# Performance work log

Hardware: AMD Instinct MI355X
Metric: run time of the kernel (lower is better)

The kernel has to match this reference:

```python
import jax, jax.numpy as jnp
import numpy as np

D_MODEL = 1024
NHEAD = 16
DK = D_MODEL // NHEAD
B, LQ, LK = 4, 2048, 2048


def setup_inputs() -> dict:
    key = jax.random.key(0)
    ks = jax.random.split(key, 11)
    s = 1.0 / np.sqrt(D_MODEL)
    inp = {
        "q": jax.random.normal(ks[0], (B, LQ, D_MODEL), jnp.float32),
        "k": jax.random.normal(ks[1], (B, LK, D_MODEL), jnp.float32),
        "v": jax.random.normal(ks[2], (B, LK, D_MODEL), jnp.float32),
        "attn_mask": jnp.triu(jnp.ones((LQ, LK), dtype=bool), k=1),  # True = masked (causal)
        "Wq": jax.random.normal(ks[3], (D_MODEL, D_MODEL), jnp.float32) * s,
        "bq": jnp.zeros((D_MODEL,), jnp.float32),
        "Wk": jax.random.normal(ks[4], (D_MODEL, D_MODEL), jnp.float32) * s,
        "bk": jnp.zeros((D_MODEL,), jnp.float32),
        "Wv": jax.random.normal(ks[5], (D_MODEL, D_MODEL), jnp.float32) * s,
        "bv": jnp.zeros((D_MODEL,), jnp.float32),
        "Wo": jax.random.normal(ks[6], (D_MODEL, D_MODEL), jnp.float32) * s,
        "bo": jnp.zeros((D_MODEL,), jnp.float32),
    }
    return inp


def _split_heads(x, L):
    # (B, L, D) -> (B, H, L, dk)
    return x.reshape(B, L, NHEAD, DK).transpose(0, 2, 1, 3)


def reference(q, k, v, attn_mask, Wq, bq, Wk, bk, Wv, bv, Wo, bo):
    qh = _split_heads(q @ Wq + bq, LQ)
    kh = _split_heads(k @ Wk + bk, LK)
    vh = _split_heads(v @ Wv + bv, LK)
    scale = 1.0 / np.sqrt(DK).astype(np.float32)
    scores = jnp.einsum("bhqd,bhkd->bhqk", qh, kh) * scale
    scores = jnp.where(attn_mask[None, None, :, :], -jnp.inf, scores)
    attn = jax.nn.softmax(scores, axis=-1)
    ctx = jnp.einsum("bhqk,bhkd->bhqd", attn, vh)
    ctx = ctx.transpose(0, 2, 1, 3).reshape(B, LQ, D_MODEL)
    return ctx @ Wo + bo
```

## Files before the change

### kernel.cpp

```cpp
#include <hip/hip_runtime.h>

#define D_MODEL 1024
#define NHEAD 16
#define DKH 64
#define BATCH 4
#define SEQ 2048
#define MROWS (BATCH*SEQ)

typedef unsigned short u16;
typedef __attribute__((ext_vector_type(8))) short bf16x8;
typedef __attribute__((ext_vector_type(4))) float f32x4;

__device__ __forceinline__ u16 f2bf(float f) {
  union { float f; unsigned int u; } x; x.f = f;
  unsigned int r = x.u + 0x7FFFu + ((x.u >> 16) & 1u);
  return (u16)(r >> 16);
}
__device__ __forceinline__ u16 f2bf_fast(float f) {
  union { float f; unsigned int u; } x; x.f = f;
  return (u16)((x.u + 0x7FFFu) >> 16);
}

__device__ __forceinline__ f32x4 mfma16(bf16x8 a, bf16x8 b, f32x4 c) {
  return __builtin_amdgcn_mfma_f32_16x16x32_bf16(a, b, c, 0, 0, 0);
}

__device__ __forceinline__ void gld_lds16(const void* g, void* l) {
  __builtin_amdgcn_global_load_lds((const __attribute__((address_space(1))) unsigned int*)g,
                                   (__attribute__((address_space(3))) unsigned int*)l, 16, 0, 0);
}

__global__ __launch_bounds__(256) void cvt3_kernel(
    const float* __restrict__ q, const float* __restrict__ k, const float* __restrict__ v,
    u16* __restrict__ oq, u16* __restrict__ ok, u16* __restrict__ ov) {
  const int seg = blockIdx.y;
  const float* in = (seg == 0) ? q : (seg == 1) ? k : v;
  u16* out = (seg == 0) ? oq : (seg == 1) ? ok : ov;
  int i = (blockIdx.x * 256 + threadIdx.x) * 4;
  float4 vv = *(const float4*)(in + i);
  ushort4 o;
  o.x = f2bf(vv.x); o.y = f2bf(vv.y); o.z = f2bf(vv.z); o.w = f2bf(vv.w);
  *(ushort4*)(out + i) = o;
}

__global__ __launch_bounds__(256) void transpose_cvt4(
    const float* __restrict__ W0, const float* __restrict__ W1,
    const float* __restrict__ W2, const float* __restrict__ W3,
    u16* __restrict__ T0, u16* __restrict__ T1,
    u16* __restrict__ T2, u16* __restrict__ T3) {
  const int z = blockIdx.z;
  const float* W = (z == 0) ? W0 : (z == 1) ? W1 : (z == 2) ? W2 : W3;
  u16* Wt = (z == 0) ? T0 : (z == 1) ? T1 : (z == 2) ? T2 : T3;
  __shared__ float tile[32][33];
  int bx = blockIdx.x * 32, by = blockIdx.y * 32;
  int tx = threadIdx.x, ty = threadIdx.y;
#pragma unroll
  for (int j = 0; j < 32; j += 8)
    tile[ty + j][tx] = W[(size_t)(by + ty + j) * D_MODEL + bx + tx];
  __syncthreads();
#pragma unroll
  for (int j = 0; j < 32; j += 8)
    Wt[(size_t)(bx + ty + j) * D_MODEL + by + tx] = f2bf(tile[tx][ty + j]);
}

template <typename Epi>
__device__ __forceinline__ void gemm_pipe(const u16* __restrict__ Ap,
                                          const u16* __restrict__ Bp,
                                          int m0, int n0g, Epi epi) {
  __shared__ u16 As[2][128 * 64];
  __shared__ u16 Bs[2][128 * 64];
  const int tid = threadIdx.x;
  const int lane = tid & 63;
  const int w = tid >> 6;
  const int wm = w >> 1, wn = w & 1;
  const int lo = lane & 15, g = lane >> 4;
  const int swz = (lo & 7) << 4;
  const int sg = (tid & 7) ^ ((tid >> 3) & 7);
  const int srow = tid >> 3;

  f32x4 acc[4][4] = {};

  auto STAGE_A = [&](int buf, int tt, int j) {
    int row = j * 32 + srow;
    gld_lds16(Ap + (size_t)(m0 + row) * D_MODEL + tt * 64 + sg * 8,
              &As[buf][j * 2048 + tid * 8]);
  };
  auto STAGE_B = [&](int buf, int tt, int j) {
    int row = j * 32 + srow;
    gld_lds16(Bp + (size_t)(n0g + row) * D_MODEL + tt * 64 + sg * 8,
              &Bs[buf][j * 2048 + tid * 8]);
  };

  STAGE_A(0, 0, 0); STAGE_A(0, 0, 1); STAGE_A(0, 0, 2); STAGE_A(0, 0, 3);
  STAGE_B(0, 0, 0); STAGE_B(0, 0, 1); STAGE_B(0, 0, 2); STAGE_B(0, 0, 3);
  STAGE_B(1, 1, 0); STAGE_B(1, 1, 1); STAGE_B(1, 1, 2); STAGE_B(1, 1, 3);
  asm volatile("s_waitcnt vmcnt(4)" ::: "memory");
  __builtin_amdgcn_s_barrier();

  int cur = 0;
#pragma unroll 1
  for (int t = 0; t < 16; ++t) {
    const int nb = cur ^ 1;
    const char* ab = (const char*)&As[cur][0];
    const char* bb2 = (const char*)&Bs[cur][0];

    bf16x8 bf[4][2], af[2][2];
#pragma unroll
    for (int n = 0; n < 4; ++n) {
      int row = wn * 64 + n * 16 + lo;
      bf[n][0] = *(const bf16x8*)(bb2 + row * 128 + ((g * 16) ^ swz));
      bf[n][1] = *(const bf16x8*)(bb2 + row * 128 + ((64 + g * 16) ^ swz));
    }
#pragma unroll
    for (int m = 0; m < 2; ++m) {
      int row = wm * 64 + m * 16 + lo;
      af[m][0] = *(const bf16x8*)(ab + row * 128 + ((g * 16) ^ swz));
      af[m][1] = *(const bf16x8*)(ab + row * 128 + ((64 + g * 16) ^ swz));
    }
    if (t + 1 < 16) {
      STAGE_A(nb, t + 1, 0); STAGE_A(nb, t + 1, 1);
      STAGE_A(nb, t + 1, 2); STAGE_A(nb, t + 1, 3);
    }
    __builtin_amdgcn_s_barrier();
    __builtin_amdgcn_s_setprio(1);
#pragma unroll
    for (int s2 = 0; s2 < 2; ++s2)
#pragma unroll
      for (int m = 0; m < 2; ++m)
#pragma unroll
        for (int n = 0; n < 4; ++n)
          acc[m][n] = mfma16(af[m][s2], bf[n][s2], acc[m][n]);
    __builtin_amdgcn_s_setprio(0);
    __builtin_amdgcn_s_barrier();

    bf16x8 af2[2][2];
#pragma unroll
    for (int m = 0; m < 2; ++m) {
      int row = wm * 64 + (m + 2) * 16 + lo;
      af2[m][0] = *(const bf16x8*)(ab + row * 128 + ((g * 16) ^ swz));
      af2[m][1] = *(const bf16x8*)(ab + row * 128 + ((64 + g * 16) ^ swz));
    }
    if (t + 2 < 16) {
      STAGE_B(cur, t + 2, 0); STAGE_B(cur, t + 2, 1);
      STAGE_B(cur, t + 2, 2); STAGE_B(cur, t + 2, 3);
    }
    __builtin_amdgcn_s_barrier();
    __builtin_amdgcn_s_setprio(1);
#pragma unroll
    for (int s2 = 0; s2 < 2; ++s2)
#pragma unroll
      for (int m = 0; m < 2; ++m)
#pragma unroll
        for (int n = 0; n < 4; ++n)
          acc[m + 2][n] = mfma16(af2[m][s2], bf[n][s2], acc[m + 2][n]);
    __builtin_amdgcn_s_setprio(0);
    if (t + 2 < 16) asm volatile("s_waitcnt vmcnt(4)" ::: "memory");
    else            asm volatile("s_waitcnt vmcnt(0)" ::: "memory");
    __builtin_amdgcn_s_barrier();
    cur = nb;
  }

  epi(acc, wm, wn, lo, g);
}

__global__ __launch_bounds__(256, 2) void gemm_qkv_kernel(
    const u16* __restrict__ Aq, const u16* __restrict__ Ak, const u16* __restrict__ Av,
    const u16* __restrict__ Wt,
    const float* __restrict__ bq, const float* __restrict__ bk, const float* __restrict__ bv,
    u16* __restrict__ Qhd, u16* __restrict__ Khd, u16* __restrict__ Vhd, float qscale) {
  const int flat = blockIdx.x;
  const int swzb = (flat & 7) * 192 + (flat >> 3);
  const int m0 = (swzb / 24) * 128;
  const int n0g = (swzb % 24) * 128;
  const int chunk = n0g >> 10;
  const u16* Ap = (chunk == 0) ? Aq : (chunk == 1) ? Ak : Av;
  const float* bias = (chunk == 0) ? bq : (chunk == 1) ? bk : bv;
  const float scale = (chunk == 0) ? qscale : 1.0f;

  gemm_pipe(Ap, Wt, m0, n0g,
    [&](f32x4 (&acc)[4][4], int wm, int wn, int lo, int g) {
#pragma unroll
      for (int m = 0; m < 4; ++m)
#pragma unroll
        for (int n = 0; n < 4; ++n) {
          int row0 = m0 + wm * 64 + m * 16 + g * 4;
          int colc = (n0g & 1023) + wn * 64 + n * 16 + lo;
          int hh = colc >> 6, d = colc & 63;
          int bb = row0 >> 11;
          float v0 = (acc[m][n][0] + bias[colc]) * scale;
          float v1 = (acc[m][n][1] + bias[colc]) * scale;
          float v2 = (acc[m][n][2] + bias[colc]) * scale;
          float v3 = (acc[m][n][3] + bias[colc]) * scale;
          if (chunk < 2) {
            u16* out = chunk ? Khd : Qhd;
#pragma unroll
            for (int i = 0; i < 4; ++i) {
              int l = (row0 + i) & 2047;
              float vi = (i == 0) ? v0 : (i == 1) ? v1 : (i == 2) ? v2 : v3;
              out[(((size_t)(bb * NHEAD + hh)) * SEQ + l) * DKH + d] = f2bf(vi);
            }
          } else {
            int l = row0 & 2047;
            int kh = (l >> 2) & 7;
            int pos = (l & ~31) | ((2 * (kh & 3) + (kh >> 2)) << 2);
            ushort4 o;
            o.x = f2bf(v0); o.y = f2bf(v1); o.z = f2bf(v2); o.w = f2bf(v3);
            *(ushort4*)&Vhd[(((size_t)(bb * NHEAD + hh)) * DKH + d) * SEQ + pos] = o;
          }
        }
    });
}

__global__ __launch_bounds__(256, 2) void gemm_o_kernel(
    const u16* __restrict__ A, const u16* __restrict__ Bt,
    const float* __restrict__ bias, float* __restrict__ Cout) {
  const int flat = blockIdx.x;
  const int swzb = (flat & 7) * 64 + (flat >> 3);
  const int m0 = (swzb >> 3) * 128;
  const int n0g = (swzb & 7) * 128;

  gemm_pipe(A, Bt, m0, n0g,
    [&](f32x4 (&acc)[4][4], int wm, int wn, int lo, int g) {
#pragma unroll
      for (int m = 0; m < 4; ++m)
#pragma unroll
        for (int n = 0; n < 4; ++n) {
          int row0 = m0 + wm * 64 + m * 16 + g * 4;
          int col = n0g + wn * 64 + n * 16 + lo;
          float bcol = bias[col];
#pragma unroll
          for (int i = 0; i < 4; ++i)
            Cout[(size_t)(row0 + i) * D_MODEL + col] = acc[m][n][i] + bcol;
        }
    });
}

__global__ __launch_bounds__(256, 3) void attn_kernel(
    const u16* __restrict__ Qh, const u16* __restrict__ Kh,
    const u16* __restrict__ Vt, u16* __restrict__ ctx) {
  const int blk = blockIdx.x;
  const int xcd = blk & 7;
  const int local = blk >> 3;
  const int qb = 15 - (local >> 3);
  const int head = xcd * 8 + (local & 7);
  const int b = head >> 4, h = head & (NHEAD - 1);

  const int tid = threadIdx.x;
  const int lane = tid & 63;
  const int w = tid >> 6;
  const int lo = lane & 15, g = lane >> 4;
  const int swz = (lo & 7) << 4;

  __shared__ u16 Ks[3][64 * 64];
  __shared__ u16 Vs[3][64 * 64];

  const size_t hoff = ((size_t)(b * NHEAD + h)) * SEQ * DKH;
  const u16* Qp = Qh + hoff;
  const u16* Kp = Kh + hoff;
  const u16* Vp = Vt + hoff;

  const int nt = 2 * qb + 2;
  const int qmin = qb * 128 + w * 32;

  bf16x8 aq[2][2];
#pragma unroll
  for (int qs = 0; qs < 2; ++qs)
#pragma unroll
    for (int cc = 0; cc < 2; ++cc)
      aq[qs][cc] = *(const bf16x8*)(Qp + (size_t)(qmin + qs * 16 + lo) * DKH + cc * 32 + g * 8);

  const int r_lo = lane >> 3;
  const int sgr = (lane & 7) ^ r_lo;

  auto STAGE = [&](int buf, int t64) {
#pragma unroll
    for (int j = 0; j < 2; ++j) {
      int row = w * 16 + j * 8 + r_lo;
      gld_lds16(Kp + (size_t)(t64 * 64 + row) * DKH + sgr * 8, &Ks[buf][(w * 2 + j) * 512]);
      gld_lds16(Vp + (size_t)row * SEQ + t64 * 64 + sgr * 8, &Vs[buf][(w * 2 + j) * 512]);
    }
  };

  STAGE(0, 0);
  STAGE(1, 1);
  asm volatile("s_waitcnt vmcnt(0)" ::: "memory");
  __builtin_amdgcn_s_barrier();

  f32x4 c[2][4] = {};
  float m_run[2] = {-1e30f, -1e30f}, l_run[2] = {0.f, 0.f};
  int cur = 0;

  for (int kt = 0; kt < nt; ++kt) {
    int b2 = cur + 2; if (b2 >= 3) b2 -= 3;
    if (kt + 2 < nt) STAGE(b2, kt + 2);

    f32x4 s[2][4] = {};
#pragma unroll
    for (int kn = 0; kn < 4; ++kn) {
      const char* krow = (const char*)&Ks[cur][(kn * 16 + lo) * 64];
#pragma unroll
      for (int cc = 0; cc < 2; ++cc) {
        bf16x8 ak = *(const bf16x8*)(krow + ((cc * 64 + g * 16) ^ swz));
        s[0][kn] = mfma16(ak, aq[0][cc], s[0][kn]);
        s[1][kn] = mfma16(ak, aq[1][cc], s[1][kn]);
      }
    }

    if (kt >= nt - 2) {
#pragma unroll
      for (int qs = 0; qs < 2; ++qs) {
        int q = qmin + qs * 16 + lo;
#pragma unroll
        for (int kn = 0; kn < 4; ++kn)
#pragma unroll
          for (int i = 0; i < 4; ++i) {
            int key = kt * 64 + kn * 16 + g * 4 + i;
            if (key > q) s[qs][kn][i] = -1e30f;
          }
      }
    }

    bf16x8 pb[2][2];
#pragma unroll
    for (int qs = 0; qs < 2; ++qs) {
      float mx = s[qs][0][0];
#pragma unroll
      for (int kn = 0; kn < 4; ++kn)
#pragma unroll
        for (int i = 0; i < 4; ++i) mx = fmaxf(mx, s[qs][kn][i]);
      mx = fmaxf(mx, __shfl_xor(mx, 16));
      mx = fmaxf(mx, __shfl_xor(mx, 32));
      float mnew = fmaxf(m_run[qs], mx);
      float al = __builtin_amdgcn_exp2f(m_run[qs] - mnew);
      m_run[qs] = mnew;
      float rs = 0.f;
#pragma unroll
      for (int kn = 0; kn < 4; ++kn)
#pragma unroll
        for (int i = 0; i < 4; ++i) {
          float p = __builtin_amdgcn_exp2f(s[qs][kn][i] - mnew);
          s[qs][kn][i] = p;
          rs += p;
        }
      rs += __shfl_xor(rs, 16);
      rs += __shfl_xor(rs, 32);
      l_run[qs] = l_run[qs] * al + rs;
#pragma unroll
      for (int dn = 0; dn < 4; ++dn) {
        c[qs][dn][0] *= al; c[qs][dn][1] *= al;
        c[qs][dn][2] *= al; c[qs][dn][3] *= al;
      }
#pragma unroll
      for (int kc = 0; kc < 2; ++kc) {
        bf16x8 t;
        t[0] = (short)f2bf_fast(s[qs][2 * kc][0]);
        t[1] = (short)f2bf_fast(s[qs][2 * kc][1]);
        t[2] = (short)f2bf_fast(s[qs][2 * kc][2]);
        t[3] = (short)f2bf_fast(s[qs][2 * kc][3]);
        t[4] = (short)f2bf_fast(s[qs][2 * kc + 1][0]);
        t[5] = (short)f2bf_fast(s[qs][2 * kc + 1][1]);
        t[6] = (short)f2bf_fast(s[qs][2 * kc + 1][2]);
        t[7] = (short)f2bf_fast(s[qs][2 * kc + 1][3]);
        pb[qs][kc] = t;
      }
    }

#pragma unroll
    for (int kc = 0; kc < 2; ++kc)
#pragma unroll
      for (int dn = 0; dn < 4; ++dn) {
        const char* vrow = (const char*)&Vs[cur][(dn * 16 + lo) * 64];
        bf16x8 av = *(const bf16x8*)(vrow + ((kc * 64 + g * 16) ^ swz));
        c[0][dn] = mfma16(av, pb[0][kc], c[0][dn]);
        c[1][dn] = mfma16(av, pb[1][kc], c[1][dn]);
      }

    if (kt + 1 < nt) {
      if (kt + 2 < nt) asm volatile("s_waitcnt vmcnt(4)" ::: "memory");
      else             asm volatile("s_waitcnt vmcnt(0)" ::: "memory");
      __builtin_amdgcn_s_barrier();
    }
    cur = (cur == 2) ? 0 : cur + 1;
  }

#pragma unroll
  for (int qs = 0; qs < 2; ++qs) {
    const float rl = 1.0f / l_run[qs];
    const int q = qmin + qs * 16 + lo;
#pragma unroll
    for (int dn = 0; dn < 4; ++dn) {
      ushort4 o;
      o.x = f2bf(c[qs][dn][0] * rl);
      o.y = f2bf(c[qs][dn][1] * rl);
      o.z = f2bf(c[qs][dn][2] * rl);
      o.w = f2bf(c[qs][dn][3] * rl);
      *(ushort4*)&ctx[((size_t)(b * SEQ + q)) * D_MODEL + h * DKH + dn * 16 + g * 4] = o;
    }
  }
}

extern "C" void kernel_launch(void* const* d_in, const int* in_sizes, int n_in,
                              void* d_out, int out_size, void* d_ws, size_t ws_size,
                              hipStream_t stream) {
  const float* q  = (const float*)d_in[0];
  const float* k  = (const float*)d_in[1];
  const float* v  = (const float*)d_in[2];
  const float* Wq = (const float*)d_in[4];
  const float* bq = (const float*)d_in[5];
  const float* Wk = (const float*)d_in[6];
  const float* bk = (const float*)d_in[7];
  const float* Wv = (const float*)d_in[8];
  const float* bv = (const float*)d_in[9];
  const float* Wo = (const float*)d_in[10];
  const float* bo = (const float*)d_in[11];

  char* ws = (char*)d_ws;
  const size_t MB = 1u << 20;
  u16* qb16 = (u16*)(ws + 0 * MB);
  u16* kb16 = (u16*)(ws + 16 * MB);
  u16* vb16 = (u16*)(ws + 32 * MB);
  u16* Wqkvt = (u16*)(ws + 48 * MB);
  u16* Wot  = (u16*)(ws + 54 * MB);
  u16* Qhd  = (u16*)(ws + 56 * MB);
  u16* Khd  = (u16*)(ws + 72 * MB);
  u16* Vhd  = (u16*)(ws + 88 * MB);
  u16* ctxb = qb16;

  cvt3_kernel<<<dim3(8192, 3), 256, 0, stream>>>(q, k, v, qb16, kb16, vb16);

  u16* Wqt = Wqkvt;
  u16* Wkt = Wqkvt + 1024 * 1024;
  u16* Wvt = Wqkvt + 2 * 1024 * 1024;
  transpose_cvt4<<<dim3(32, 32, 4), dim3(32, 8), 0, stream>>>(
      Wq, Wk, Wv, Wo, Wqt, Wkt, Wvt, Wot);

  const float qscale = 0.125f * 1.4426950408889634f;
  gemm_qkv_kernel<<<1536, 256, 0, stream>>>(qb16, kb16, vb16, Wqkvt,
                                            bq, bk, bv, Qhd, Khd, Vhd, qscale);

  attn_kernel<<<1024, 256, 0, stream>>>(Qhd, Khd, Vhd, ctxb);

  gemm_o_kernel<<<512, 256, 0, stream>>>(ctxb, Wot, bo, (float*)d_out);
}
```

Baseline: 177.4 us.

## Load GEMM B operand from global directly, shrink LDS buffers, add lazy softmax rescale

New measurement: 313.3 us. +76.6%, slower.

```diff
diff --git a/kernel.cpp b/kernel.cpp
--- a/kernel.cpp
+++ b/kernel.cpp
@@ -15,10 +15,6 @@
   union { float f; unsigned int u; } x; x.f = f;
   unsigned int r = x.u + 0x7FFFu + ((x.u >> 16) & 1u);
   return (u16)(r >> 16);
-}
-__device__ __forceinline__ u16 f2bf_fast(float f) {
-  union { float f; unsigned int u; } x; x.f = f;
-  return (u16)((x.u + 0x7FFFu) >> 16);
 }
 
 __device__ __forceinline__ f32x4 mfma16(bf16x8 a, bf16x8 b, f32x4 c) {
@@ -64,106 +60,76 @@
 }
 
 template <typename Epi>
-__device__ __forceinline__ void gemm_pipe(const u16* __restrict__ Ap,
-                                          const u16* __restrict__ Bp,
-                                          int m0, int n0g, Epi epi) {
+__device__ __forceinline__ void gemm_bg(const u16* __restrict__ Ap,
+                                        const u16* __restrict__ Bp,
+                                        int m0, int n0g, Epi epi) {
   __shared__ u16 As[2][128 * 64];
-  __shared__ u16 Bs[2][128 * 64];
   const int tid = threadIdx.x;
   const int lane = tid & 63;
   const int w = tid >> 6;
   const int wm = w >> 1, wn = w & 1;
   const int lo = lane & 15, g = lane >> 4;
   const int swz = (lo & 7) << 4;
-  const int sg = (tid & 7) ^ ((tid >> 3) & 7);
   const int srow = tid >> 3;
+  const int sgr = (tid & 7) ^ (srow & 7);
 
   f32x4 acc[4][4] = {};
 
-  auto STAGE_A = [&](int buf, int tt, int j) {
-    int row = j * 32 + srow;
-    gld_lds16(Ap + (size_t)(m0 + row) * D_MODEL + tt * 64 + sg * 8,
-              &As[buf][j * 2048 + tid * 8]);
+  auto STAGE_A = [&](int buf, int tt) {
+#pragma unroll
+    for (int j = 0; j < 4; ++j)
+      gld_lds16(Ap + (size_t)(m0 + j * 32 + srow) * D_MODEL + tt * 64 + sgr * 8,
+                &As[buf][j * 2048 + tid * 8]);
   };
-  auto STAGE_B = [&](int buf, int tt, int j) {
-    int row = j * 32 + srow;
-    gld_lds16(Bp + (size_t)(n0g + row) * D_MODEL + tt * 64 + sg * 8,
-              &Bs[buf][j * 2048 + tid * 8]);
-  };
-
-  STAGE_A(0, 0, 0); STAGE_A(0, 0, 1); STAGE_A(0, 0, 2); STAGE_A(0, 0, 3);
-  STAGE_B(0, 0, 0); STAGE_B(0, 0, 1); STAGE_B(0, 0, 2); STAGE_B(0, 0, 3);
-  STAGE_B(1, 1, 0); STAGE_B(1, 1, 1); STAGE_B(1, 1, 2); STAGE_B(1, 1, 3);
-  asm volatile("s_waitcnt vmcnt(4)" ::: "memory");
+
+  const u16* brow[4];
+#pragma unroll
+  for (int n = 0; n < 4; ++n)
+    brow[n] = Bp + (size_t)(n0g + wn * 64 + n * 16 + lo) * D_MODEL;
+
+  STAGE_A(0, 0);
+  asm volatile("s_waitcnt vmcnt(0)" ::: "memory");
   __builtin_amdgcn_s_barrier();
 
-  int cur = 0;
 #pragma unroll 1
   for (int t = 0; t < 16; ++t) {
-    const int nb = cur ^ 1;
+    const int cur = t & 1;
+    bf16x8 b0[4], b1[4];
+#pragma unroll
+    for (int n = 0; n < 4; ++n) b0[n] = *(const bf16x8*)(brow[n] + t * 64 + g * 8);
+#pragma unroll
+    for (int n = 0; n < 4; ++n) b1[n] = *(const bf16x8*)(brow[n] + t * 64 + 32 + g * 8);
+    if (t + 1 < 16) STAGE_A(cur ^ 1, t + 1);
     const char* ab = (const char*)&As[cur][0];
-    const char* bb2 = (const char*)&Bs[cur][0];
-
-    bf16x8 bf[4][2], af[2][2];
-#pragma unroll
-    for (int n = 0; n < 4; ++n) {
-      int row = wn * 64 + n * 16 + lo;
-      bf[n][0] = *(const bf16x8*)(bb2 + row * 128 + ((g * 16) ^ swz));
-      bf[n][1] = *(const bf16x8*)(bb2 + row * 128 + ((64 + g * 16) ^ swz));
-    }
-#pragma unroll
-    for (int m = 0; m < 2; ++m) {
-      int row = wm * 64 + m * 16 + lo;
-      af[m][0] = *(const bf16x8*)(ab + row * 128 + ((g * 16) ^ swz));
-      af[m][1] = *(const bf16x8*)(ab + row * 128 + ((64 + g * 16) ^ swz));
-    }
+    bf16x8 a0[4], a1[4];
+#pragma unroll
+    for (int m = 0; m < 4; ++m)
+      a0[m] = *(const bf16x8*)(ab + (wm * 64 + m * 16 + lo) * 128 + ((g * 16) ^ swz));
+#pragma unroll
+    for (int m = 0; m < 4; ++m)
+      a1[m] = *(const bf16x8*)(ab + (wm * 64 + m * 16 + lo) * 128 + ((64 + g * 16) ^ swz));
+    __builtin_amdgcn_s_setprio(1);
+#pragma unroll
+    for (int m = 0; m < 4; ++m)
+#pragma unroll
+      for (int n = 0; n < 4; ++n)
+        acc[m][n] = mfma16(a0[m], b0[n], acc[m][n]);
+#pragma unroll
+    for (int m = 0; m < 4; ++m)
+#pragma unroll
+      for (int n = 0; n < 4; ++n)
+        acc[m][n] = mfma16(a1[m], b1[n], acc[m][n]);
+    __builtin_amdgcn_s_setprio(0);
     if (t + 1 < 16) {
-      STAGE_A(nb, t + 1, 0); STAGE_A(nb, t + 1, 1);
-      STAGE_A(nb, t + 1, 2); STAGE_A(nb, t + 1, 3);
-    }
-    __builtin_amdgcn_s_barrier();
-    __builtin_amdgcn_s_setprio(1);
-#pragma unroll
-    for (int s2 = 0; s2 < 2; ++s2)
-#pragma unroll
-      for (int m = 0; m < 2; ++m)
-#pragma unroll
-        for (int n = 0; n < 4; ++n)
-          acc[m][n] = mfma16(af[m][s2], bf[n][s2], acc[m][n]);
-    __builtin_amdgcn_s_setprio(0);
-    __builtin_amdgcn_s_barrier();
-
-    bf16x8 af2[2][2];
-#pragma unroll
-    for (int m = 0; m < 2; ++m) {
-      int row = wm * 64 + (m + 2) * 16 + lo;
-      af2[m][0] = *(const bf16x8*)(ab + row * 128 + ((g * 16) ^ swz));
-      af2[m][1] = *(const bf16x8*)(ab + row * 128 + ((64 + g * 16) ^ swz));
-    }
-    if (t + 2 < 16) {
-      STAGE_B(cur, t + 2, 0); STAGE_B(cur, t + 2, 1);
-      STAGE_B(cur, t + 2, 2); STAGE_B(cur, t + 2, 3);
-    }
-    __builtin_amdgcn_s_barrier();
-    __builtin_amdgcn_s_setprio(1);
-#pragma unroll
-    for (int s2 = 0; s2 < 2; ++s2)
-#pragma unroll
-      for (int m = 0; m < 2; ++m)
-#pragma unroll
-        for (int n = 0; n < 4; ++n)
-          acc[m + 2][n] = mfma16(af2[m][s2], bf[n][s2], acc[m + 2][n]);
-    __builtin_amdgcn_s_setprio(0);
-    if (t + 2 < 16) asm volatile("s_waitcnt vmcnt(4)" ::: "memory");
-    else            asm volatile("s_waitcnt vmcnt(0)" ::: "memory");
-    __builtin_amdgcn_s_barrier();
-    cur = nb;
+      asm volatile("s_waitcnt vmcnt(0)" ::: "memory");
+      __builtin_amdgcn_sched_barrier(0);
+      __builtin_amdgcn_s_barrier();
+    }
   }
-
   epi(acc, wm, wn, lo, g);
 }
 
-__global__ __launch_bounds__(256, 2) void gemm_qkv_kernel(
+__global__ __launch_bounds__(256, 3) void gemm_qkv_kernel(
     const u16* __restrict__ Aq, const u16* __restrict__ Ak, const u16* __restrict__ Av,
     const u16* __restrict__ Wt,
     const float* __restrict__ bq, const float* __restrict__ bk, const float* __restrict__ bv,
@@ -177,7 +143,7 @@
   const float* bias = (chunk == 0) ? bq : (chunk == 1) ? bk : bv;
   const float scale = (chunk == 0) ? qscale : 1.0f;
 
-  gemm_pipe(Ap, Wt, m0, n0g,
+  gemm_bg(Ap, Wt, m0, n0g,
     [&](f32x4 (&acc)[4][4], int wm, int wn, int lo, int g) {
 #pragma unroll
       for (int m = 0; m < 4; ++m)
@@ -211,7 +177,7 @@
     });
 }
 
-__global__ __launch_bounds__(256, 2) void gemm_o_kernel(
+__global__ __launch_bounds__(256, 3) void gemm_o_kernel(
     const u16* __restrict__ A, const u16* __restrict__ Bt,
     const float* __restrict__ bias, float* __restrict__ Cout) {
   const int flat = blockIdx.x;
@@ -219,7 +185,7 @@
   const int m0 = (swzb >> 3) * 128;
   const int n0g = (swzb & 7) * 128;
 
-  gemm_pipe(A, Bt, m0, n0g,
+  gemm_bg(A, Bt, m0, n0g,
     [&](f32x4 (&acc)[4][4], int wm, int wn, int lo, int g) {
 #pragma unroll
       for (int m = 0; m < 4; ++m)
@@ -235,7 +201,7 @@
     });
 }
 
-__global__ __launch_bounds__(256, 3) void attn_kernel(
+__global__ __launch_bounds__(256, 5) void attn_kernel(
     const u16* __restrict__ Qh, const u16* __restrict__ Kh,
     const u16* __restrict__ Vt, u16* __restrict__ ctx) {
   const int blk = blockIdx.x;
@@ -251,8 +217,8 @@
   const int lo = lane & 15, g = lane >> 4;
   const int swz = (lo & 7) << 4;
 
-  __shared__ u16 Ks[3][64 * 64];
-  __shared__ u16 Vs[3][64 * 64];
+  __shared__ u16 Ks[2][64 * 64];
+  __shared__ u16 Vs[2][64 * 64];
 
   const size_t hoff = ((size_t)(b * NHEAD + h)) * SEQ * DKH;
   const u16* Qp = Qh + hoff;
@@ -282,17 +248,15 @@
   };
 
   STAGE(0, 0);
-  STAGE(1, 1);
   asm volatile("s_waitcnt vmcnt(0)" ::: "memory");
   __builtin_amdgcn_s_barrier();
 
   f32x4 c[2][4] = {};
   float m_run[2] = {-1e30f, -1e30f}, l_run[2] = {0.f, 0.f};
-  int cur = 0;
 
   for (int kt = 0; kt < nt; ++kt) {
-    int b2 = cur + 2; if (b2 >= 3) b2 -= 3;
-    if (kt + 2 < nt) STAGE(b2, kt + 2);
+    const int cur = kt & 1;
+    if (kt + 1 < nt) STAGE(cur ^ 1, kt + 1);
 
     f32x4 s[2][4] = {};
 #pragma unroll
@@ -330,38 +294,40 @@
         for (int i = 0; i < 4; ++i) mx = fmaxf(mx, s[qs][kn][i]);
       mx = fmaxf(mx, __shfl_xor(mx, 16));
       mx = fmaxf(mx, __shfl_xor(mx, 32));
-      float mnew = fmaxf(m_run[qs], mx);
-      float al = __builtin_amdgcn_exp2f(m_run[qs] - mnew);
-      m_run[qs] = mnew;
+      if (!__all(mx - m_run[qs] <= 8.0f)) {
+        float mnew = fmaxf(m_run[qs], mx);
+        float al = __builtin_amdgcn_exp2f(m_run[qs] - mnew);
+        m_run[qs] = mnew;
+        l_run[qs] *= al;
+#pragma unroll
+        for (int dn = 0; dn < 4; ++dn) {
+          c[qs][dn][0] *= al; c[qs][dn][1] *= al;
+          c[qs][dn][2] *= al; c[qs][dn][3] *= al;
+        }
+      }
+      const float mq = m_run[qs];
       float rs = 0.f;
 #pragma unroll
       for (int kn = 0; kn < 4; ++kn)
 #pragma unroll
         for (int i = 0; i < 4; ++i) {
-          float p = __builtin_amdgcn_exp2f(s[qs][kn][i] - mnew);
+          float p = __builtin_amdgcn_exp2f(s[qs][kn][i] - mq);
           s[qs][kn][i] = p;
           rs += p;
         }
       rs += __shfl_xor(rs, 16);
       rs += __shfl_xor(rs, 32);
-      l_run[qs] = l_run[qs] * al + rs;
-#pragma unroll
-      for (int dn = 0; dn < 4; ++dn) {
-        c[qs][dn][0] *= al; c[qs][dn][1] *= al;
-        c[qs][dn][2] *= al; c[qs][dn][3] *= al;
-      }
+      l_run[qs] += rs;
 #pragma unroll
       for (int kc = 0; kc < 2; ++kc) {
-        bf16x8 t;
-        t[0] = (short)f2bf_fast(s[qs][2 * kc][0]);
-        t[1] = (short)f2bf_fast(s[qs][2 * kc][1]);
-        t[2] = (short)f2bf_fast(s[qs][2 * kc][2]);
-        t[3] = (short)f2bf_fast(s[qs][2 * kc][3]);
-        t[4] = (short)f2bf_fast(s[qs][2 * kc + 1][0]);
-        t[5] = (short)f2bf_fast(s[qs][2 * kc + 1][1]);
-        t[6] = (short)f2bf_fast(s[qs][2 * kc + 1][2]);
-        t[7] = (short)f2bf_fast(s[qs][2 * kc + 1][3]);
-        pb[qs][kc] = t;
+        unsigned int u0, u1, u2, u3;
+        asm("v_cvt_pk_bf16_f32 %0, %1, %2" : "=v"(u0) : "v"(s[qs][2 * kc][0]), "v"(s[qs][2 * kc][1]));
+        asm("v_cvt_pk_bf16_f32 %0, %1, %2" : "=v"(u1) : "v"(s[qs][2 * kc][2]), "v"(s[qs][2 * kc][3]));
+        asm("v_cvt_pk_bf16_f32 %0, %1, %2" : "=v"(u2) : "v"(s[qs][2 * kc + 1][0]), "v"(s[qs][2 * kc + 1][1]));
+        asm("v_cvt_pk_bf16_f32 %0, %1, %2" : "=v"(u3) : "v"(s[qs][2 * kc + 1][2]), "v"(s[qs][2 * kc + 1][3]));
+        union { unsigned int u[4]; bf16x8 v8; } pk;
+        pk.u[0] = u0; pk.u[1] = u1; pk.u[2] = u2; pk.u[3] = u3;
+        pb[qs][kc] = pk.v8;
       }
     }
 
@@ -376,11 +342,10 @@
       }
 
     if (kt + 1 < nt) {
-      if (kt + 2 < nt) asm volatile("s_waitcnt vmcnt(4)" ::: "memory");
-      else             asm volatile("s_waitcnt vmcnt(0)" ::: "memory");
+      asm volatile("s_waitcnt vmcnt(0)" ::: "memory");
+      __builtin_amdgcn_sched_barrier(0);
       __builtin_amdgcn_s_barrier();
     }
-    cur = (cur == 2) ? 0 : cur + 1;
   }
 
 #pragma unroll
```
